# Performance work log

Measured on AMD Instinct MI355X. Metric: run time of the kernel, lower is better.

## Reference

```python
import jax, jax.numpy as jnp
import numpy as np

B, N, C, H = 8, 1024, 768, 12
D = C // H  # head_dim = 64
SCALE = D ** -0.5


def setup_inputs() -> dict:
    key = jax.random.key(0)
    ks = jax.random.split(key, 5)
    s = lambda k, sh, fan: jax.random.normal(k, sh, jnp.float32) * (fan ** -0.5)
    return {
        "x": jax.random.normal(ks[0], (B, N, C), jnp.float32),
        "w_qkv": s(ks[1], (C, 3 * C), C),
        "b_qkv": jnp.zeros((3 * C,), jnp.float32),
        "w_l": s(ks[2], (H, H), H),
        "b_l": jnp.zeros((H,), jnp.float32),
        "w_w": s(ks[3], (H, H), H),
        "b_w": jnp.zeros((H,), jnp.float32),
        "w_proj": s(ks[4], (C, C), C),
        "b_proj": jnp.zeros((C,), jnp.float32),
    }


def reference(x, w_qkv, b_qkv, w_l, b_l, w_w, b_w, w_proj, b_proj):
    Bq, Nq, Cq = x.shape
    # qkv projection -> (3, B, H, N, D)
    qkv = (x @ w_qkv + b_qkv).reshape(Bq, Nq, 3, H, D).transpose(2, 0, 3, 1, 4)
    q, k, v = qkv[0] * SCALE, qkv[1], qkv[2]
    # raw scores [B, H, N, N]
    attn = jnp.einsum("bhnd,bhmd->bhnm", q, k)
    # pre-softmax talking-heads: mix across head axis (Dense over H)
    attn = jnp.einsum("bhnm,hg->bgnm", attn, w_l) + b_l[None, :, None, None]
    attn = jax.nn.softmax(attn, axis=-1)
    # post-softmax talking-heads
    attn = jnp.einsum("bhnm,hg->bgnm", attn, w_w) + b_w[None, :, None, None]
    # weighted values -> (B, N, C)
    out = jnp.einsum("bhnm,bhmd->bnhd", attn, v).reshape(Bq, Nq, Cq)
    return out @ w_proj + b_proj
```

## Files before the change

### kernel.cpp

```cpp
#include <hip/hip_runtime.h>

#define BB 8
#define NN 1024
#define CC 768
#define HH 12
#define DD 64

typedef unsigned short u16;
typedef unsigned int u32;
typedef __attribute__((ext_vector_type(8))) short s16x8;
typedef __attribute__((ext_vector_type(4))) short s16x4;
typedef __attribute__((ext_vector_type(4))) float f32x4;
typedef __attribute__((ext_vector_type(2))) u32 u32x2;
typedef __attribute__((ext_vector_type(4))) u32 u32x4;

__device__ __forceinline__ float bf2f(u16 u) {
  u32 x = ((u32)u) << 16;
  return __builtin_bit_cast(float, x);
}
__device__ __forceinline__ u16 f2bf(float f) {
  u32 x = __builtin_bit_cast(u32, f);
  x += 0x7fffu + ((x >> 16) & 1u);
  return (u16)(x >> 16);
}
__device__ __forceinline__ float hw_exp2(float x) { return __builtin_amdgcn_exp2f(x); }
__device__ __forceinline__ float hw_log2(float x) { return __builtin_amdgcn_logf(x); }
__device__ __forceinline__ s16x8 lds_read8(const u16* p) {
  u32x2 a = *(const u32x2*)p;
  u32x2 b = *(const u32x2*)(p + 4);
  u32x4 m = {a.x, a.y, b.x, b.y};
  return __builtin_bit_cast(s16x8, m);
}

__global__ __launch_bounds__(256) void convx_kernel(const float* __restrict__ in,
                                                    u16* __restrict__ out) {
  size_t i = ((size_t)blockIdx.x * 256 + threadIdx.x) * 8;
  f32x4 a = *(const f32x4*)(in + i);
  f32x4 b = *(const f32x4*)(in + i + 4);
  s16x8 r;
#pragma unroll
  for (int j = 0; j < 4; j++) { r[j] = (short)f2bf(a[j]); r[4 + j] = (short)f2bf(b[j]); }
  *(s16x8*)(out + i) = r;
}

__global__ __launch_bounds__(256) void transpose_kernel(const float* __restrict__ in,
                                                        u16* __restrict__ out,
                                                        int R, int C) {
  __shared__ float t[32][33];
  const int cl = threadIdx.x & 31, rq = threadIdx.x >> 5;
#pragma unroll
  for (int rr = 0; rr < 4; rr++) {
    int rl = rq * 4 + rr;
    t[rl][cl] = in[(size_t)(blockIdx.y * 32 + rl) * C + blockIdx.x * 32 + cl];
  }
  __syncthreads();
#pragma unroll
  for (int rr = 0; rr < 4; rr++) {
    int oc = rq * 4 + rr;
    out[(size_t)(blockIdx.x * 32 + oc) * R + blockIdx.y * 32 + cl] = f2bf(t[cl][oc]);
  }
}

__global__ __launch_bounds__(256) void qkv_gemm(
    const u16* __restrict__ A, const u16* __restrict__ Bt, const float* __restrict__ bias,
    u16* __restrict__ qo, u16* __restrict__ ko, u16* __restrict__ vo) {
  __shared__ __align__(16) u16 As[128 * 32];
  __shared__ __align__(16) u16 Bs[128 * 32];
  const int tid = threadIdx.x;
  const int w = tid >> 6, lane = tid & 63, l15 = lane & 15, l4 = lane >> 4;
  const int wm = w & 1, wn = w >> 1;
  const int m0 = blockIdx.x * 128, n0 = blockIdx.y * 128;
  const int sr = lane >> 2, sk = (lane & 3) * 8;

  f32x4 acc[4][4];
#pragma unroll
  for (int a = 0; a < 4; a++)
#pragma unroll
    for (int bb = 0; bb < 4; bb++) acc[a][bb] = (f32x4){0.f, 0.f, 0.f, 0.f};

  for (int k0 = 0; k0 < CC; k0 += 32) {
    s16x8 a0 = *(const s16x8*)(A + (size_t)(m0 + w * 16 + sr) * CC + k0 + sk);
    s16x8 a1 = *(const s16x8*)(A + (size_t)(m0 + 64 + w * 16 + sr) * CC + k0 + sk);
    s16x8 b0 = *(const s16x8*)(Bt + (size_t)(n0 + w * 16 + sr) * CC + k0 + sk);
    s16x8 b1 = *(const s16x8*)(Bt + (size_t)(n0 + 64 + w * 16 + sr) * CC + k0 + sk);
    __syncthreads();
    *(s16x8*)&As[(w * 16 + sr) * 32 + sk] = a0;
    *(s16x8*)&As[(64 + w * 16 + sr) * 32 + sk] = a1;
    *(s16x8*)&Bs[(w * 16 + sr) * 32 + sk] = b0;
    *(s16x8*)&Bs[(64 + w * 16 + sr) * 32 + sk] = b1;
    __syncthreads();
    s16x8 af[4], bf[4];
#pragma unroll
    for (int a = 0; a < 4; a++) af[a] = *(const s16x8*)&As[(wm * 64 + a * 16 + l15) * 32 + l4 * 8];
#pragma unroll
    for (int bb = 0; bb < 4; bb++) bf[bb] = *(const s16x8*)&Bs[(wn * 64 + bb * 16 + l15) * 32 + l4 * 8];
#pragma unroll
    for (int a = 0; a < 4; a++)
#pragma unroll
      for (int bb = 0; bb < 4; bb++)
        acc[a][bb] = __builtin_amdgcn_mfma_f32_16x16x32_bf16(af[a], bf[bb], acc[a][bb], 0, 0, 0);
  }

  const int b = (m0 >> 10);
#pragma unroll
  for (int bb = 0; bb < 4; bb++) {
    int col = n0 + wn * 64 + bb * 16 + l15;
    int s = col / CC;
    int rem = col - s * CC;
    int h = rem >> 6, d = rem & 63;
    float bv = bias[col];
#pragma unroll
    for (int a = 0; a < 4; a++) {
      int row0 = m0 + wm * 64 + a * 16 + l4 * 4;
      int nt0 = row0 & (NN - 1);
      if (s == 2) {
        s16x4 pk;
#pragma unroll
        for (int r = 0; r < 4; r++) pk[r] = (short)f2bf(acc[a][bb][r] + bv);
        *(s16x4*)(vo + (((size_t)((b * HH + h) * DD + d)) << 10) + nt0) = pk;
      } else if (s == 0) {
#pragma unroll
        for (int r = 0; r < 4; r++)
          qo[(((size_t)((b * HH + h) * NN + nt0 + r)) << 6) + d] = f2bf((acc[a][bb][r] + bv) * 0.125f);
      } else {
#pragma unroll
        for (int r = 0; r < 4; r++)
          ko[(((size_t)((b * HH + h) * NN + nt0 + r)) << 6) + d] = f2bf(acc[a][bb][r] + bv);
      }
    }
  }
}

__global__ __launch_bounds__(256) void proj_gemm(
    const u16* __restrict__ A, const u16* __restrict__ Bt, const float* __restrict__ bias,
    float* __restrict__ out) {
  __shared__ __align__(16) u16 As[128 * 32];
  __shared__ __align__(16) u16 Bs[128 * 32];
  const int tid = threadIdx.x;
  const int w = tid >> 6, lane = tid & 63, l15 = lane & 15, l4 = lane >> 4;
  const int wm = w & 1, wn = w >> 1;
  const int m0 = blockIdx.x * 128, n0 = blockIdx.y * 128;
  const int sr = lane >> 2, sk = (lane & 3) * 8;

  f32x4 acc[4][4];
#pragma unroll
  for (int a = 0; a < 4; a++)
#pragma unroll
    for (int bb = 0; bb < 4; bb++) acc[a][bb] = (f32x4){0.f, 0.f, 0.f, 0.f};

  for (int k0 = 0; k0 < CC; k0 += 32) {
    s16x8 a0 = *(const s16x8*)(A + (size_t)(m0 + w * 16 + sr) * CC + k0 + sk);
    s16x8 a1 = *(const s16x8*)(A + (size_t)(m0 + 64 + w * 16 + sr) * CC + k0 + sk);
    s16x8 b0 = *(const s16x8*)(Bt + (size_t)(n0 + w * 16 + sr) * CC + k0 + sk);
    s16x8 b1 = *(const s16x8*)(Bt + (size_t)(n0 + 64 + w * 16 + sr) * CC + k0 + sk);
    __syncthreads();
    *(s16x8*)&As[(w * 16 + sr) * 32 + sk] = a0;
    *(s16x8*)&As[(64 + w * 16 + sr) * 32 + sk] = a1;
    *(s16x8*)&Bs[(w * 16 + sr) * 32 + sk] = b0;
    *(s16x8*)&Bs[(64 + w * 16 + sr) * 32 + sk] = b1;
    __syncthreads();
    s16x8 af[4], bf[4];
#pragma unroll
    for (int a = 0; a < 4; a++) af[a] = *(const s16x8*)&As[(wm * 64 + a * 16 + l15) * 32 + l4 * 8];
#pragma unroll
    for (int bb = 0; bb < 4; bb++) bf[bb] = *(const s16x8*)&Bs[(wn * 64 + bb * 16 + l15) * 32 + l4 * 8];
#pragma unroll
    for (int a = 0; a < 4; a++)
#pragma unroll
      for (int bb = 0; bb < 4; bb++)
        acc[a][bb] = __builtin_amdgcn_mfma_f32_16x16x32_bf16(af[a], bf[bb], acc[a][bb], 0, 0, 0);
  }

#pragma unroll
  for (int bb = 0; bb < 4; bb++) {
    int col = n0 + wn * 64 + bb * 16 + l15;
    float bv = bias[col];
#pragma unroll
    for (int a = 0; a < 4; a++) {
      int row0 = m0 + wm * 64 + a * 16 + l4 * 4;
#pragma unroll
      for (int r = 0; r < 4; r++)
        out[(size_t)(row0 + r) * CC + col] = acc[a][bb][r] + bv;
    }
  }
}

#define SB_BYTES 28736
#define UT_OFF   SB_BYTES
#define UT_ELE   6912
#define LL2_OFF  (SB_BYTES + 27648)
#define SM_TOTAL (LL2_OFF + 1088)

__global__ __launch_bounds__(512, 4) void attn_kernel(
    const u16* __restrict__ qg, const u16* __restrict__ kg, const u16* __restrict__ vtg,
    const float* __restrict__ wlg, const float* __restrict__ blg,
    const float* __restrict__ wwg, const float* __restrict__ bwg,
    u16* __restrict__ aout) {
  __shared__ __align__(16) char smem[SM_TOTAL];
  u16* Sb = (u16*)smem;
  u16* Ut0 = (u16*)(smem + UT_OFF);
  float* lpart = (float*)(smem + UT_OFF);
  float* ll2 = (float*)(smem + LL2_OFF);

  const int b = blockIdx.x, i0 = blockIdx.y * 16;
  const int tid = threadIdx.x;
  const int w = tid >> 6, lane = tid & 63, l15 = lane & 15, l4 = lane >> 4;
  const float RLN2 = 1.44269504088896340736f;

  for (int j = tid; j < SB_BYTES / 4; j += 512) ((u32*)smem)[j] = 0;

  s16x8 wlS, wlA1, wlA2, wwA1, wwA2;
#pragma unroll
  for (int j = 0; j < 8; j++) {
    int k = l4 * 8 + j;
    float v1 = (k < 12 && l15 < 12) ? wlg[k * 12 + l15] * RLN2 : 0.f;
    wlS[j] = (short)f2bf(v1);
    int h = k >> 1, pt = k & 1;
    float v2 = (h < 12 && l15 < 12) ? wlg[h * 12 + l15] * RLN2 : 0.f;
    u16 h2 = f2bf(v2); u16 lo2 = f2bf(v2 - bf2f(h2));
    wlA1[j] = (short)h2; wlA2[j] = (short)(pt ? 0 : lo2);
    float v3 = (h < 12 && l15 < 12) ? wwg[h * 12 + l15] : 0.f;
    u16 h3 = f2bf(v3); u16 lo3 = f2bf(v3 - bf2f(h3));
    wwA1[j] = (short)h3; wwA2[j] = (short)(pt ? 0 : lo3);
  }
  int gr[4]; float blv[4], bwv[4];
#pragma unroll
  for (int r = 0; r < 4; r++) {
    gr[r] = l4 * 4 + r;
    blv[r] = (gr[r] < 12) ? blg[gr[r]] * RLN2 : 0.f;
    bwv[r] = (gr[r] < 12) ? bwg[gr[r]] : 0.f;
  }

  int jh[3], jmb[3];
  s16x8 qf[3][2];
#pragma unroll
  for (int jt = 0; jt < 3; jt++) {
    int j = w * 3 + jt;
    jh[jt] = j % 12; jmb[jt] = j / 12;
    const u16* qp = qg + (((size_t)((b * HH + jh[jt]) * NN + i0 + l15)) << 6) + l4 * 8;
    qf[jt][0] = *(const s16x8*)qp;
    qf[jt][1] = *(const s16x8*)(qp + 32);
  }

  float la[4] = {0.f, 0.f, 0.f, 0.f};
  for (int mt = 0; mt < 32; mt++) {
    const int m0 = mt * 32;
#pragma unroll
    for (int jt = 0; jt < 3; jt++) {
      f32x4 c = (f32x4){0.f, 0.f, 0.f, 0.f};
      const u16* kp = kg + (((size_t)((b * HH + jh[jt]) * NN + m0 + jmb[jt] * 16 + l15)) << 6) + l4 * 8;
      c = __builtin_amdgcn_mfma_f32_16x16x32_bf16(*(const s16x8*)kp, qf[jt][0], c, 0, 0, 0);
      c = __builtin_amdgcn_mfma_f32_16x16x32_bf16(*(const s16x8*)(kp + 32), qf[jt][1], c, 0, 0, 0);
      int cb = (jmb[jt] * 16 + l4 * 4) * 16 + l15;
#pragma unroll
      for (int r = 0; r < 4; r++)
        Sb[(size_t)(cb + r * 16) * 20 + jh[jt]] = f2bf(c[r]);
    }
    __syncthreads();
#pragma unroll
    for (int tt = 0; tt < 4; tt++) {
      int t = w * 4 + tt;
      s16x8 bS = lds_read8(Sb + (size_t)(t * 16 + l15) * 20 + l4 * 8);
      f32x4 T = (f32x4){blv[0], blv[1], blv[2], blv[3]};
      T = __builtin_amdgcn_mfma_f32_16x16x32_bf16(wlS, bS, T, 0, 0, 0);
#pragma unroll
      for (int r = 0; r < 4; r++) la[r] += hw_exp2(T[r]);
    }
    __syncthreads();
  }

#pragma unroll
  for (int r = 0; r < 4; r++) lpart[w * 256 + gr[r] * 16 + l15] = la[r];
  __syncthreads();
  if (tid < 256) {
    float s = 0.f;
#pragma unroll
    for (int w2 = 0; w2 < 8; w2++) s += lpart[w2 * 256 + tid];
    ll2[(tid >> 4) * 17 + (tid & 15)] = hw_log2(s);
  }
  __syncthreads();
  float Tinit[4];
#pragma unroll
  for (int r = 0; r < 4; r++) Tinit[r] = blv[r] - ll2[gr[r] * 17 + l15];

  const int db = w >> 1, pvh = (w & 1) * 6;
  f32x4 O[6];
#pragma unroll
  for (int jp = 0; jp < 6; jp++) O[jp] = (f32x4){0.f, 0.f, 0.f, 0.f};

  for (int mt = 0; mt < 32; mt++) {
    const int m0 = mt * 32;
    u16* Utb = Ut0 + (mt & 1) * UT_ELE;
#pragma unroll
    for (int jt = 0; jt < 3; jt++) {
      f32x4 c = (f32x4){0.f, 0.f, 0.f, 0.f};
      const u16* kp = kg + (((size_t)((b * HH + jh[jt]) * NN + m0 + jmb[jt] * 16 + l15)) << 6) + l4 * 8;
      c = __builtin_amdgcn_mfma_f32_16x16x32_bf16(*(const s16x8*)kp, qf[jt][0], c, 0, 0, 0);
      c = __builtin_amdgcn_mfma_f32_16x16x32_bf16(*(const s16x8*)(kp + 32), qf[jt][1], c, 0, 0, 0);
      int cb = (jmb[jt] * 16 + l4 * 4) * 16 + l15;
#pragma unroll
      for (int r = 0; r < 4; r++) {
        float v = c[r];
        u32 xv = __builtin_bit_cast(u32, v);
        float hf = __builtin_bit_cast(float, xv & 0xFFFF0000u);
        u16 lo = f2bf(v - hf);
        *(u32*)(Sb + (size_t)(cb + r * 16) * 28 + 2 * jh[jt]) = (xv >> 16) | ((u32)lo << 16);
      }
    }
    __syncthreads();
#pragma unroll
    for (int tt = 0; tt < 4; tt++) {
      int t = w * 4 + tt;
      s16x8 bS = lds_read8(Sb + (size_t)(t * 16 + l15) * 28 + l4 * 8);
      f32x4 T = (f32x4){Tinit[0], Tinit[1], Tinit[2], Tinit[3]};
      T = __builtin_amdgcn_mfma_f32_16x16x32_bf16(wlA1, bS, T, 0, 0, 0);
      T = __builtin_amdgcn_mfma_f32_16x16x32_bf16(wlA2, bS, T, 0, 0, 0);
      u32x4 pk;
#pragma unroll
      for (int r = 0; r < 4; r++) {
        float P = hw_exp2(T[r]);
        u32 xp = __builtin_bit_cast(u32, P);
        float hf = __builtin_bit_cast(float, xp & 0xFFFF0000u);
        u16 lo = f2bf(P - hf);
        pk[r] = (xp >> 16) | ((u32)lo << 16);
      }
      s16x8 bP = __builtin_bit_cast(s16x8, pk);
      f32x4 U = (f32x4){bwv[0], bwv[1], bwv[2], bwv[3]};
      U = __builtin_amdgcn_mfma_f32_16x16x32_bf16(wwA1, bP, U, 0, 0, 0);
      U = __builtin_amdgcn_mfma_f32_16x16x32_bf16(wwA2, bP, U, 0, 0, 0);
#pragma unroll
      for (int r = 0; r < 4; r++)
        if (gr[r] < 12) Utb[(size_t)(gr[r] * 16 + l15) * 36 + t] = f2bf(U[r]);
    }
    __syncthreads();
#pragma unroll
    for (int jp = 0; jp < 6; jp++) {
      const int h = pvh + jp;
      s16x8 aV = *(const s16x8*)(vtg + (((size_t)((b * HH + h) * DD + db * 16 + l15)) << 10) + m0 + l4 * 8);
      s16x8 bU = lds_read8(Utb + (size_t)(h * 16 + l15) * 36 + l4 * 8);
      O[jp] = __builtin_amdgcn_mfma_f32_16x16x32_bf16(aV, bU, O[jp], 0, 0, 0);
    }
  }

#pragma unroll
  for (int jp = 0; jp < 6; jp++) {
    const int h = pvh + jp;
    const int d0 = db * 16 + l4 * 4;
    s16x4 pk4;
#pragma unroll
    for (int r = 0; r < 4; r++) pk4[r] = (short)f2bf(O[jp][r]);
    *(s16x4*)(aout + ((size_t)(b * NN) + i0 + l15) * CC + h * DD + d0) = pk4;
  }
}

extern "C" void kernel_launch(void* const* d_in, const int* in_sizes, int n_in,
                              void* d_out, int out_size, void* d_ws, size_t ws_size,
                              hipStream_t stream) {
  const float* x      = (const float*)d_in[0];
  const float* w_qkv  = (const float*)d_in[1];
  const float* b_qkv  = (const float*)d_in[2];
  const float* w_l    = (const float*)d_in[3];
  const float* b_l    = (const float*)d_in[4];
  const float* w_w    = (const float*)d_in[5];
  const float* b_w    = (const float*)d_in[6];
  const float* w_proj = (const float*)d_in[7];
  const float* b_proj = (const float*)d_in[8];

  const size_t per = (size_t)BB * HH * NN * DD;
  u16* xb  = (u16*)d_ws;
  u16* wqt = xb + per;
  u16* wpt = wqt + (size_t)3 * CC * CC;
  u16* q   = wpt + (size_t)CC * CC;
  u16* k   = q + per;
  u16* vt  = k + per;
  u16* ao  = vt + per;

  convx_kernel<<<3072, 256, 0, stream>>>(x, xb);
  transpose_kernel<<<dim3(3 * CC / 32, CC / 32), 256, 0, stream>>>(w_qkv, wqt, CC, 3 * CC);
  transpose_kernel<<<dim3(CC / 32, CC / 32), 256, 0, stream>>>(w_proj, wpt, CC, CC);
  qkv_gemm<<<dim3(64, 18), 256, 0, stream>>>(xb, wqt, b_qkv, q, k, vt);
  attn_kernel<<<dim3(BB, NN / 16), 512, 0, stream>>>(q, k, vt, w_l, b_l, w_w, b_w, ao);
  proj_gemm<<<dim3(64, 6), 256, 0, stream>>>(ao, wpt, b_proj, (float*)d_out);
}
```

Measured before the change: 448.7 us.

## Pipeline PV step one tile behind, double-buffer first-pass scores, use direct-to-LDS GEMM loads

The attention second pass now runs the PV MFMA for the previous key tile while the current tile's scores and U are computed. This removes one barrier per iteration and uses s_setprio to favour the MFMAs. The first (log-sum) pass double-buffers its score LDS tile so the trailing barrier can go, and lpart moves to its own region. Both GEMMs replace register-staged global-to-LDS copies with global_load_lds direct loads. This changes the wave-to-row mapping and relies on the LDS layout produced by the intrinsic. A packhl helper replaces the split-bf16 packing with a truncation of the low part instead of rounding.

```diff
diff --git a/kernel.cpp b/kernel.cpp
--- a/kernel.cpp
+++ b/kernel.cpp
@@ -30,6 +30,16 @@
   u32x2 b = *(const u32x2*)(p + 4);
   u32x4 m = {a.x, a.y, b.x, b.y};
   return __builtin_bit_cast(s16x8, m);
+}
+__device__ __forceinline__ u32 packhl(float v) {
+  u32 xv = __builtin_bit_cast(u32, v);
+  float lo = v - __builtin_bit_cast(float, xv & 0xFFFF0000u);
+  return (xv >> 16) | (__builtin_bit_cast(u32, lo) & 0xFFFF0000u);
+}
+__device__ __forceinline__ void gload_lds16(const u16* g, u16* l) {
+  __builtin_amdgcn_global_load_lds(
+      (const __attribute__((address_space(1))) u32*)g,
+      (__attribute__((address_space(3))) u32*)l, 16, 0, 0);
 }
 
 __global__ __launch_bounds__(256) void convx_kernel(const float* __restrict__ in,
@@ -70,7 +80,7 @@
   const int w = tid >> 6, lane = tid & 63, l15 = lane & 15, l4 = lane >> 4;
   const int wm = w & 1, wn = w >> 1;
   const int m0 = blockIdx.x * 128, n0 = blockIdx.y * 128;
-  const int sr = lane >> 2, sk = (lane & 3) * 8;
+  const int grow = lane >> 2, gcol = (lane & 3) * 8;
 
   f32x4 acc[4][4];
 #pragma unroll
@@ -79,15 +89,13 @@
     for (int bb = 0; bb < 4; bb++) acc[a][bb] = (f32x4){0.f, 0.f, 0.f, 0.f};
 
   for (int k0 = 0; k0 < CC; k0 += 32) {
-    s16x8 a0 = *(const s16x8*)(A + (size_t)(m0 + w * 16 + sr) * CC + k0 + sk);
-    s16x8 a1 = *(const s16x8*)(A + (size_t)(m0 + 64 + w * 16 + sr) * CC + k0 + sk);
-    s16x8 b0 = *(const s16x8*)(Bt + (size_t)(n0 + w * 16 + sr) * CC + k0 + sk);
-    s16x8 b1 = *(const s16x8*)(Bt + (size_t)(n0 + 64 + w * 16 + sr) * CC + k0 + sk);
-    __syncthreads();
-    *(s16x8*)&As[(w * 16 + sr) * 32 + sk] = a0;
-    *(s16x8*)&As[(64 + w * 16 + sr) * 32 + sk] = a1;
-    *(s16x8*)&Bs[(w * 16 + sr) * 32 + sk] = b0;
-    *(s16x8*)&Bs[(64 + w * 16 + sr) * 32 + sk] = b1;
+    __syncthreads();
+    const u16* ga = A + (size_t)(m0 + w * 32 + grow) * CC + k0 + gcol;
+    const u16* gb = Bt + (size_t)(n0 + w * 32 + grow) * CC + k0 + gcol;
+    gload_lds16(ga, &As[w * 1024]);
+    gload_lds16(ga + (size_t)16 * CC, &As[w * 1024 + 512]);
+    gload_lds16(gb, &Bs[w * 1024]);
+    gload_lds16(gb + (size_t)16 * CC, &Bs[w * 1024 + 512]);
     __syncthreads();
     s16x8 af[4], bf[4];
 #pragma unroll
@@ -140,7 +148,7 @@
   const int w = tid >> 6, lane = tid & 63, l15 = lane & 15, l4 = lane >> 4;
   const int wm = w & 1, wn = w >> 1;
   const int m0 = blockIdx.x * 128, n0 = blockIdx.y * 128;
-  const int sr = lane >> 2, sk = (lane & 3) * 8;
+  const int grow = lane >> 2, gcol = (lane & 3) * 8;
 
   f32x4 acc[4][4];
 #pragma unroll
@@ -149,15 +157,13 @@
     for (int bb = 0; bb < 4; bb++) acc[a][bb] = (f32x4){0.f, 0.f, 0.f, 0.f};
 
   for (int k0 = 0; k0 < CC; k0 += 32) {
-    s16x8 a0 = *(const s16x8*)(A + (size_t)(m0 + w * 16 + sr) * CC + k0 + sk);
-    s16x8 a1 = *(const s16x8*)(A + (size_t)(m0 + 64 + w * 16 + sr) * CC + k0 + sk);
-    s16x8 b0 = *(const s16x8*)(Bt + (size_t)(n0 + w * 16 + sr) * CC + k0 + sk);
-    s16x8 b1 = *(const s16x8*)(Bt + (size_t)(n0 + 64 + w * 16 + sr) * CC + k0 + sk);
-    __syncthreads();
-    *(s16x8*)&As[(w * 16 + sr) * 32 + sk] = a0;
-    *(s16x8*)&As[(64 + w * 16 + sr) * 32 + sk] = a1;
-    *(s16x8*)&Bs[(w * 16 + sr) * 32 + sk] = b0;
-    *(s16x8*)&Bs[(64 + w * 16 + sr) * 32 + sk] = b1;
+    __syncthreads();
+    const u16* ga = A + (size_t)(m0 + w * 32 + grow) * CC + k0 + gcol;
+    const u16* gb = Bt + (size_t)(n0 + w * 32 + grow) * CC + k0 + gcol;
+    gload_lds16(ga, &As[w * 1024]);
+    gload_lds16(ga + (size_t)16 * CC, &As[w * 1024 + 512]);
+    gload_lds16(gb, &Bs[w * 1024]);
+    gload_lds16(gb + (size_t)16 * CC, &Bs[w * 1024 + 512]);
     __syncthreads();
     s16x8 af[4], bf[4];
 #pragma unroll
@@ -185,11 +191,13 @@
   }
 }
 
-#define SB_BYTES 28736
-#define UT_OFF   SB_BYTES
-#define UT_ELE   6912
-#define LL2_OFF  (SB_BYTES + 27648)
-#define SM_TOTAL (LL2_OFF + 1088)
+#define SB2_BYTES 28736
+#define UT_OFF    SB2_BYTES
+#define UT_ELE    6912
+#define SB1_U16   10272
+#define LPART_OFF 48192
+#define LL2_OFF   56384
+#define SM_TOTAL  (LL2_OFF + 1088)
 
 __global__ __launch_bounds__(512, 4) void attn_kernel(
     const u16* __restrict__ qg, const u16* __restrict__ kg, const u16* __restrict__ vtg,
@@ -198,8 +206,9 @@
     u16* __restrict__ aout) {
   __shared__ __align__(16) char smem[SM_TOTAL];
   u16* Sb = (u16*)smem;
+  u16* Sb1 = (u16*)smem;
   u16* Ut0 = (u16*)(smem + UT_OFF);
-  float* lpart = (float*)(smem + UT_OFF);
+  float* lpart = (float*)(smem + LPART_OFF);
   float* ll2 = (float*)(smem + LL2_OFF);
 
   const int b = blockIdx.x, i0 = blockIdx.y * 16;
@@ -207,7 +216,8 @@
   const int w = tid >> 6, lane = tid & 63, l15 = lane & 15, l4 = lane >> 4;
   const float RLN2 = 1.44269504088896340736f;
 
-  for (int j = tid; j < SB_BYTES / 4; j += 512) ((u32*)smem)[j] = 0;
+  for (int j = tid; j < 10272; j += 512) ((u32*)smem)[j] = 0;
+  __syncthreads();
 
   s16x8 wlS, wlA1, wlA2, wwA1, wwA2;
 #pragma unroll
@@ -245,6 +255,7 @@
   float la[4] = {0.f, 0.f, 0.f, 0.f};
   for (int mt = 0; mt < 32; mt++) {
     const int m0 = mt * 32;
+    u16* Sp = Sb1 + (mt & 1) * SB1_U16;
 #pragma unroll
     for (int jt = 0; jt < 3; jt++) {
       f32x4 c = (f32x4){0.f, 0.f, 0.f, 0.f};
@@ -254,19 +265,18 @@
       int cb = (jmb[jt] * 16 + l4 * 4) * 16 + l15;
 #pragma unroll
       for (int r = 0; r < 4; r++)
-        Sb[(size_t)(cb + r * 16) * 20 + jh[jt]] = f2bf(c[r]);
+        Sp[(size_t)(cb + r * 16) * 20 + jh[jt]] = f2bf(c[r]);
     }
     __syncthreads();
 #pragma unroll
     for (int tt = 0; tt < 4; tt++) {
       int t = w * 4 + tt;
-      s16x8 bS = lds_read8(Sb + (size_t)(t * 16 + l15) * 20 + l4 * 8);
+      s16x8 bS = lds_read8(Sp + (size_t)(t * 16 + l15) * 20 + l4 * 8);
       f32x4 T = (f32x4){blv[0], blv[1], blv[2], blv[3]};
       T = __builtin_amdgcn_mfma_f32_16x16x32_bf16(wlS, bS, T, 0, 0, 0);
 #pragma unroll
       for (int r = 0; r < 4; r++) la[r] += hw_exp2(T[r]);
     }
-    __syncthreads();
   }
 
 #pragma unroll
@@ -287,10 +297,20 @@
   f32x4 O[6];
 #pragma unroll
   for (int jp = 0; jp < 6; jp++) O[jp] = (f32x4){0.f, 0.f, 0.f, 0.f};
+  s16x8 aV[6], bU[6];
 
   for (int mt = 0; mt < 32; mt++) {
     const int m0 = mt * 32;
-    u16* Utb = Ut0 + (mt & 1) * UT_ELE;
+    u16* Utw = Ut0 + (mt & 1) * UT_ELE;
+    const u16* Utr = Ut0 + ((mt & 1) ^ 1) * UT_ELE;
+
+    if (mt > 0) {
+#pragma unroll
+      for (int jp = 0; jp < 6; jp++) {
+        const int h = pvh + jp;
+        aV[jp] = *(const s16x8*)(vtg + (((size_t)((b * HH + h) * DD + db * 16 + l15)) << 10) + (m0 - 32) + l4 * 8);
+      }
+    }
 #pragma unroll
     for (int jt = 0; jt < 3; jt++) {
       f32x4 c = (f32x4){0.f, 0.f, 0.f, 0.f};
@@ -299,15 +319,15 @@
       c = __builtin_amdgcn_mfma_f32_16x16x32_bf16(*(const s16x8*)(kp + 32), qf[jt][1], c, 0, 0, 0);
       int cb = (jmb[jt] * 16 + l4 * 4) * 16 + l15;
 #pragma unroll
-      for (int r = 0; r < 4; r++) {
-        float v = c[r];
-        u32 xv = __builtin_bit_cast(u32, v);
-        float hf = __builtin_bit_cast(float, xv & 0xFFFF0000u);
-        u16 lo = f2bf(v - hf);
-        *(u32*)(Sb + (size_t)(cb + r * 16) * 28 + 2 * jh[jt]) = (xv >> 16) | ((u32)lo << 16);
-      }
-    }
-    __syncthreads();
+      for (int r = 0; r < 4; r++)
+        *(u32*)(Sb + (size_t)(cb + r * 16) * 28 + 2 * jh[jt]) = packhl(c[r]);
+    }
+    __syncthreads();
+    if (mt > 0) {
+#pragma unroll
+      for (int jp = 0; jp < 6; jp++)
+        bU[jp] = lds_read8(Utr + (size_t)((pvh + jp) * 16 + l15) * 36 + l4 * 8);
+    }
 #pragma unroll
     for (int tt = 0; tt < 4; tt++) {
       int t = w * 4 + tt;
@@ -317,28 +337,32 @@
       T = __builtin_amdgcn_mfma_f32_16x16x32_bf16(wlA2, bS, T, 0, 0, 0);
       u32x4 pk;
 #pragma unroll
-      for (int r = 0; r < 4; r++) {
-        float P = hw_exp2(T[r]);
-        u32 xp = __builtin_bit_cast(u32, P);
-        float hf = __builtin_bit_cast(float, xp & 0xFFFF0000u);
-        u16 lo = f2bf(P - hf);
-        pk[r] = (xp >> 16) | ((u32)lo << 16);
-      }
+      for (int r = 0; r < 4; r++) pk[r] = packhl(hw_exp2(T[r]));
       s16x8 bP = __builtin_bit_cast(s16x8, pk);
       f32x4 U = (f32x4){bwv[0], bwv[1], bwv[2], bwv[3]};
       U = __builtin_amdgcn_mfma_f32_16x16x32_bf16(wwA1, bP, U, 0, 0, 0);
       U = __builtin_amdgcn_mfma_f32_16x16x32_bf16(wwA2, bP, U, 0, 0, 0);
 #pragma unroll
       for (int r = 0; r < 4; r++)
-        if (gr[r] < 12) Utb[(size_t)(gr[r] * 16 + l15) * 36 + t] = f2bf(U[r]);
-    }
-    __syncthreads();
+        if (gr[r] < 12) Utw[(size_t)(gr[r] * 16 + l15) * 36 + t] = f2bf(U[r]);
+    }
+    if (mt > 0) {
+      __builtin_amdgcn_s_setprio(1);
+#pragma unroll
+      for (int jp = 0; jp < 6; jp++)
+        O[jp] = __builtin_amdgcn_mfma_f32_16x16x32_bf16(aV[jp], bU[jp], O[jp], 0, 0, 0);
+      __builtin_amdgcn_s_setprio(0);
+    }
+    __syncthreads();
+  }
+  {
+    const u16* Utr = Ut0 + UT_ELE;
 #pragma unroll
     for (int jp = 0; jp < 6; jp++) {
       const int h = pvh + jp;
-      s16x8 aV = *(const s16x8*)(vtg + (((size_t)((b * HH + h) * DD + db * 16 + l15)) << 10) + m0 + l4 * 8);
-      s16x8 bU = lds_read8(Utb + (size_t)(h * 16 + l15) * 36 + l4 * 8);
-      O[jp] = __builtin_amdgcn_mfma_f32_16x16x32_bf16(aV, bU, O[jp], 0, 0, 0);
+      s16x8 aVe = *(const s16x8*)(vtg + (((size_t)((b * HH + h) * DD + db * 16 + l15)) << 10) + 31 * 32 + l4 * 8);
+      s16x8 bUe = lds_read8(Utr + (size_t)(h * 16 + l15) * 36 + l4 * 8);
+      O[jp] = __builtin_amdgcn_mfma_f32_16x16x32_bf16(aVe, bUe, O[jp], 0, 0, 0);
     }
   }
 
```

After: 664.9 us. 48.2% more time.
